# Kernel optimization log

Hardware: AMD Instinct MI355X
Metric: run time of the kernel (lower is better)

## Reference

```python
import jax, jax.numpy as jnp
import numpy as np

B, SQ, SKV, D = 32, 1024, 8192, 64

def setup_inputs() -> dict:
    key = jax.random.key(0)
    kq, kk, kv = jax.random.split(key, 3)
    return {
        "q_local": jax.random.normal(kq, (B, SQ, D), dtype=jnp.float32),
        "k_local": jax.random.normal(kk, (B, SKV, D), dtype=jnp.float32),
        "v_local": jax.random.normal(kv, (B, SKV, D), dtype=jnp.float32),
    }

def reference(q_local, k_local, v_local):
    # Ring attention with online softmax over all ranks' K/V blocks is
    # mathematically identical to unscaled softmax(Q K^T) V over the full KV.
    scores = jnp.einsum("bqd,bkd->bqk", q_local, k_local)  # [B, SQ, SKV]
    weights = jax.nn.softmax(scores, axis=-1)              # stable (max-subtract)
    out = jnp.einsum("bqk,bkd->bqd", weights, v_local)
    return out.astype(q_local.dtype)
```

## Files before the change

### kernel.cpp

```cpp
#include <hip/hip_runtime.h>


#define NBATCH 32
#define SQL 1024
#define SKVL 8192
#define DH 64
#define BM 128
#define BN 64
#define KSTR 72
#define VSTR 72

typedef _Float16 half8 __attribute__((ext_vector_type(8)));
typedef __fp16 fp16x2 __attribute__((ext_vector_type(2)));
typedef float floatx16 __attribute__((ext_vector_type(16)));
typedef float floatx4 __attribute__((ext_vector_type(4)));
typedef unsigned int uint4v __attribute__((ext_vector_type(4)));
typedef unsigned int uint2v __attribute__((ext_vector_type(2)));

union F8U { uint4v u; half8 h; };

#if __has_builtin(__builtin_amdgcn_exp2f)
#define EXP2F(x) __builtin_amdgcn_exp2f(x)
#else
#define EXP2F(x) exp2f(x)
#endif

static __device__ __forceinline__ unsigned pk2(float a, float b) {
#if __has_builtin(__builtin_amdgcn_cvt_pkrtz)
  fp16x2 h = __builtin_amdgcn_cvt_pkrtz(a, b);
  return __builtin_bit_cast(unsigned, h);
#else
  union { _Float16 h[2]; unsigned u; } r;
  r.h[0] = (_Float16)a; r.h[1] = (_Float16)b; return r.u;
#endif
}

#if __has_builtin(__builtin_amdgcn_permlane32_swap)
#define HAVE_PL32 1
static __device__ __forceinline__ void pl32(unsigned& a, unsigned& b) {
  uint2v r = __builtin_amdgcn_permlane32_swap(a, b, false, false);
  a = r[0]; b = r[1];
}
#else
#define HAVE_PL32 0
#endif

template<int NSPLIT>
__global__ __launch_bounds__(256, 3)
void ring_attn(const float* __restrict__ q, const float* __restrict__ k,
               const float* __restrict__ v, float* __restrict__ out,
               float* __restrict__ pO, float* __restrict__ pM, float* __restrict__ pL)
{
  constexpr int NT = SKVL / NSPLIT / BN;
  __shared__ _Float16 Kl[2][BN * KSTR];
  __shared__ _Float16 Vt[2][DH * VSTR];

  const int tid  = threadIdx.x;
  const int lane = tid & 63;
  const int wv   = tid >> 6;
  const int l31  = lane & 31;
  const int hb   = lane >> 5;
  const int b8   = hb * 8;

  int split, batch, qb;
  if (NSPLIT == 4) {
    split = blockIdx.x & 3;
    batch = (blockIdx.x >> 2) & 31;
    qb    = blockIdx.x >> 7;
  } else {
    split = 0;
    batch = blockIdx.x & 31;
    qb    = blockIdx.x >> 5;
  }

  const float* kp = k + ((size_t)batch * SKVL + (size_t)split * (SKVL / NSPLIT)) * DH;
  const float* vp = v + ((size_t)batch * SKVL + (size_t)split * (SKVL / NSPLIT)) * DH;

  const float* qp = q + ((size_t)batch * SQL + qb * BM + wv * 32 + l31) * DH;
  half8 qf[4];
#pragma unroll
  for (int kt = 0; kt < 4; ++kt) {
    float4 a = *(const float4*)(qp + kt * 16 + b8);
    float4 c = *(const float4*)(qp + kt * 16 + b8 + 4);
    float xs[8] = {a.x, a.y, a.z, a.w, c.x, c.y, c.z, c.w};
#pragma unroll
    for (int j = 0; j < 8; ++j)
      qf[kt][j] = (_Float16)(xs[j] * 1.44269504088896340736f);
  }

  const int krt = tid >> 4;
  const int kc  = (tid & 15) * 4;
  const int vnr = 2 * (tid & 31);
  const int vcg = 8 * (tid >> 5);

  float4 gk[4], ga0, ga1, gb0, gb1;
#pragma unroll
  for (int it = 0; it < 4; ++it)
    gk[it] = *(const float4*)(kp + (size_t)(krt + it * 16) * DH + kc);
  ga0 = *(const float4*)(vp + (size_t)vnr * DH + vcg);
  ga1 = *(const float4*)(vp + (size_t)vnr * DH + vcg + 4);
  gb0 = *(const float4*)(vp + (size_t)(vnr + 1) * DH + vcg);
  gb1 = *(const float4*)(vp + (size_t)(vnr + 1) * DH + vcg + 4);

  floatx16 accO[2];
#pragma unroll
  for (int i = 0; i < 2; ++i)
#pragma unroll
    for (int r = 0; r < 16; ++r) accO[i][r] = 0.f;
  float m_run = -3.0e38f, l_run = 0.f;

  int buf = 0;
  for (int tile = 0; tile < NT; ++tile) {
    _Float16* Kb = Kl[buf];
    _Float16* Vb = Vt[buf];

#pragma unroll
    for (int it = 0; it < 4; ++it) {
      uint2 w2 = make_uint2(pk2(gk[it].x, gk[it].y), pk2(gk[it].z, gk[it].w));
      *(uint2*)&Kb[(krt + it * 16) * KSTR + kc] = w2;
    }
    {
      float av[8] = {ga0.x, ga0.y, ga0.z, ga0.w, ga1.x, ga1.y, ga1.z, ga1.w};
      float bv[8] = {gb0.x, gb0.y, gb0.z, gb0.w, gb1.x, gb1.y, gb1.z, gb1.w};
#pragma unroll
      for (int i = 0; i < 8; ++i)
        *(unsigned*)&Vb[(vcg + i) * VSTR + vnr] = pk2(av[i], bv[i]);
    }
    __syncthreads();

    if (tile + 1 < NT) {
      const float* kn = kp + (size_t)(tile + 1) * BN * DH;
      const float* vn = vp + (size_t)(tile + 1) * BN * DH;
#pragma unroll
      for (int it = 0; it < 4; ++it)
        gk[it] = *(const float4*)(kn + (size_t)(krt + it * 16) * DH + kc);
      ga0 = *(const float4*)(vn + (size_t)vnr * DH + vcg);
      ga1 = *(const float4*)(vn + (size_t)vnr * DH + vcg + 4);
      gb0 = *(const float4*)(vn + (size_t)(vnr + 1) * DH + vcg);
      gb1 = *(const float4*)(vn + (size_t)(vnr + 1) * DH + vcg + 4);
    }

    floatx16 st[2];
#pragma unroll
    for (int t = 0; t < 2; ++t)
#pragma unroll
      for (int r = 0; r < 16; ++r) st[t][r] = 0.f;
#pragma unroll
    for (int kt = 0; kt < 4; ++kt) {
#pragma unroll
      for (int t = 0; t < 2; ++t) {
        half8 kf = *(const half8*)&Kb[(t * 32 + l31) * KSTR + kt * 16 + b8];
        st[t] = __builtin_amdgcn_mfma_f32_32x32x16_f16(kf, qf[kt], st[t], 0, 0, 0);
      }
    }

    float mx = -3.0e38f;
#pragma unroll
    for (int t = 0; t < 2; ++t)
#pragma unroll
      for (int r = 0; r < 16; ++r) mx = fmaxf(mx, st[t][r]);
    mx = fmaxf(mx, __shfl_xor(mx, 32, 64));
    float m_new = fmaxf(m_run, mx);
    float alpha = EXP2F(m_run - m_new);
    m_run = m_new;
    float sum = 0.f;
#pragma unroll
    for (int t = 0; t < 2; ++t)
#pragma unroll
      for (int r = 0; r < 16; ++r) {
        float p = EXP2F(st[t][r] - m_new);
        st[t][r] = p;
        sum += p;
      }
    sum += __shfl_xor(sum, 32, 64);
    l_run = alpha * l_run + sum;

    if (__any(alpha != 1.0f)) {
#pragma unroll
      for (int r = 0; r < 16; ++r) {
        int row = (r & 3) + 8 * (r >> 2) + 4 * hb;
        float ar = __shfl(alpha, row, 64);
        accO[0][r] *= ar;
        accO[1][r] *= ar;
      }
    }

#pragma unroll
    for (int t = 0; t < 2; ++t) {
      unsigned P01 = pk2(st[t][0],  st[t][1]);
      unsigned P23 = pk2(st[t][2],  st[t][3]);
      unsigned P45 = pk2(st[t][4],  st[t][5]);
      unsigned P67 = pk2(st[t][6],  st[t][7]);
      unsigned P89 = pk2(st[t][8],  st[t][9]);
      unsigned PAB = pk2(st[t][10], st[t][11]);
      unsigned PCD = pk2(st[t][12], st[t][13]);
      unsigned PEF = pk2(st[t][14], st[t][15]);
      F8U fe, fo;
#if HAVE_PL32
      pl32(P01, P45); fe.u[0] = P01; fe.u[2] = P45;
      pl32(P23, P67); fe.u[1] = P23; fe.u[3] = P67;
      pl32(P89, PCD); fo.u[0] = P89; fo.u[2] = PCD;
      pl32(PAB, PEF); fo.u[1] = PAB; fo.u[3] = PEF;
#else
      unsigned x01 = __shfl_xor(P01, 32, 64), x23 = __shfl_xor(P23, 32, 64);
      unsigned x45 = __shfl_xor(P45, 32, 64), x67 = __shfl_xor(P67, 32, 64);
      unsigned x89 = __shfl_xor(P89, 32, 64), xAB = __shfl_xor(PAB, 32, 64);
      unsigned xCD = __shfl_xor(PCD, 32, 64), xEF = __shfl_xor(PEF, 32, 64);
      fe.u = uint4v{hb ? x45 : P01, hb ? x67 : P23, hb ? P45 : x01, hb ? P67 : x23};
      fo.u = uint4v{hb ? xCD : P89, hb ? xEF : PAB, hb ? PCD : x89, hb ? PEF : xAB};
#endif
#pragma unroll
      for (int ds = 0; ds < 2; ++ds) {
        half8 vf0 = *(const half8*)&Vb[(ds * 32 + l31) * VSTR + (2 * t) * 16 + b8];
        accO[ds] = __builtin_amdgcn_mfma_f32_32x32x16_f16(fe.h, vf0, accO[ds], 0, 0, 0);
        half8 vf1 = *(const half8*)&Vb[(ds * 32 + l31) * VSTR + (2 * t + 1) * 16 + b8];
        accO[ds] = __builtin_amdgcn_mfma_f32_32x32x16_f16(fo.h, vf1, accO[ds], 0, 0, 0);
      }
    }
    buf ^= 1;
  }

  const int rowbase = batch * SQL + qb * BM + wv * 32;
  if (NSPLIT == 1) {
    float linv = 1.0f / l_run;
    float* op = out + (size_t)rowbase * DH;
#pragma unroll
    for (int r = 0; r < 16; ++r) {
      int row = (r & 3) + 8 * (r >> 2) + 4 * hb;
      float lr = __shfl(linv, row, 64);
      op[(size_t)row * DH + l31]      = accO[0][r] * lr;
      op[(size_t)row * DH + 32 + l31] = accO[1][r] * lr;
    }
  } else {
    float* po = pO + ((size_t)split * NBATCH * SQL + rowbase) * DH;
#pragma unroll
    for (int r = 0; r < 16; ++r) {
      int row = (r & 3) + 8 * (r >> 2) + 4 * hb;
      po[(size_t)row * DH + l31]      = accO[0][r];
      po[(size_t)row * DH + 32 + l31] = accO[1][r];
    }
    if (hb == 0) {
      pM[(size_t)split * NBATCH * SQL + rowbase + l31] = m_run;
      pL[(size_t)split * NBATCH * SQL + rowbase + l31] = l_run;
    }
  }
}

__global__ __launch_bounds__(256)
void merge4(const float* __restrict__ pO, const float* __restrict__ pM,
            const float* __restrict__ pL, float* __restrict__ out)
{
  const int i4   = blockIdx.x * 256 + threadIdx.x;
  const int rowg = i4 >> 4;
  const size_t PLANE4 = (size_t)NBATCH * SQL * DH / 4;
  const int    RPL    = NBATCH * SQL;
  float m0 = pM[rowg], m1 = pM[RPL + rowg], m2 = pM[2 * RPL + rowg], m3 = pM[3 * RPL + rowg];
  float mx = fmaxf(fmaxf(m0, m1), fmaxf(m2, m3));
  float w0 = EXP2F(m0 - mx), w1 = EXP2F(m1 - mx), w2 = EXP2F(m2 - mx), w3 = EXP2F(m3 - mx);
  float l = w0 * pL[rowg] + w1 * pL[RPL + rowg] + w2 * pL[2 * RPL + rowg] + w3 * pL[3 * RPL + rowg];
  float li = 1.0f / l;
  const floatx4* p0 = (const floatx4*)pO;
  floatx4 o0 = p0[i4], o1 = p0[PLANE4 + i4], o2 = p0[2 * PLANE4 + i4], o3 = p0[3 * PLANE4 + i4];
  floatx4 o;
#pragma unroll
  for (int j = 0; j < 4; ++j)
    o[j] = (w0 * o0[j] + w1 * o1[j] + w2 * o2[j] + w3 * o3[j]) * li;
  ((floatx4*)out)[i4] = o;
}

extern "C" void kernel_launch(void* const* d_in, const int* in_sizes, int n_in,
                              void* d_out, int out_size, void* d_ws, size_t ws_size,
                              hipStream_t stream) {
  (void)in_sizes; (void)n_in; (void)out_size;
  const float* q = (const float*)d_in[0];
  const float* k = (const float*)d_in[1];
  const float* v = (const float*)d_in[2];
  float* out = (float*)d_out;

  const size_t PLANE = (size_t)NBATCH * SQL * DH;
  const size_t RPL   = (size_t)NBATCH * SQL;
  const size_t need  = (4 * PLANE + 8 * RPL) * sizeof(float);

  if (ws_size >= need) {
    float* pO = (float*)d_ws;
    float* pM = pO + 4 * PLANE;
    float* pL = pM + 4 * RPL;
    ring_attn<4><<<dim3(1024), dim3(256), 0, stream>>>(q, k, v, nullptr, pO, pM, pL);
    merge4<<<dim3((NBATCH * SQL * DH) / 1024), dim3(256), 0, stream>>>(pO, pM, pL, out);
  } else {
    ring_attn<1><<<dim3(256), dim3(256), 0, stream>>>(q, k, v, out, nullptr, nullptr, nullptr);
  }
}
```

Before: 250.9 us.

## Split tile barrier so V stores overlap QK MFMAs, add setprio and tree reductions

New measurement: 245.2 us. -2.3%, faster.

```diff
diff --git a/kernel.cpp b/kernel.cpp
--- a/kernel.cpp
+++ b/kernel.cpp
@@ -24,6 +24,12 @@
 #else
 #define EXP2F(x) exp2f(x)
 #endif
+
+#define WGBAR() do {                                        \
+    asm volatile("s_waitcnt lgkmcnt(0)" ::: "memory");      \
+    __builtin_amdgcn_s_barrier();                           \
+    asm volatile("" ::: "memory");                          \
+  } while (0)
 
 static __device__ __forceinline__ unsigned pk2(float a, float b) {
 #if __has_builtin(__builtin_amdgcn_cvt_pkrtz)
@@ -119,6 +125,8 @@
       uint2 w2 = make_uint2(pk2(gk[it].x, gk[it].y), pk2(gk[it].z, gk[it].w));
       *(uint2*)&Kb[(krt + it * 16) * KSTR + kc] = w2;
     }
+    WGBAR();
+
     {
       float av[8] = {ga0.x, ga0.y, ga0.z, ga0.w, ga1.x, ga1.y, ga1.z, ga1.w};
       float bv[8] = {gb0.x, gb0.y, gb0.z, gb0.w, gb1.x, gb1.y, gb1.z, gb1.w};
@@ -126,7 +134,6 @@
       for (int i = 0; i < 8; ++i)
         *(unsigned*)&Vb[(vcg + i) * VSTR + vnr] = pk2(av[i], bv[i]);
     }
-    __syncthreads();
 
     if (tile + 1 < NT) {
       const float* kn = kp + (size_t)(tile + 1) * BN * DH;
@@ -145,6 +152,7 @@
     for (int t = 0; t < 2; ++t)
 #pragma unroll
       for (int r = 0; r < 16; ++r) st[t][r] = 0.f;
+    __builtin_amdgcn_s_setprio(1);
 #pragma unroll
     for (int kt = 0; kt < 4; ++kt) {
 #pragma unroll
@@ -153,26 +161,34 @@
         st[t] = __builtin_amdgcn_mfma_f32_32x32x16_f16(kf, qf[kt], st[t], 0, 0, 0);
       }
     }
-
-    float mx = -3.0e38f;
-#pragma unroll
-    for (int t = 0; t < 2; ++t)
-#pragma unroll
-      for (int r = 0; r < 16; ++r) mx = fmaxf(mx, st[t][r]);
-    mx = fmaxf(mx, __shfl_xor(mx, 32, 64));
+    __builtin_amdgcn_s_setprio(0);
+
+    float red[16];
+#pragma unroll
+    for (int r = 0; r < 16; ++r) red[r] = fmaxf(st[0][r], st[1][r]);
+#pragma unroll
+    for (int s = 8; s >= 1; s >>= 1)
+#pragma unroll
+      for (int r = 0; r < 8; ++r)
+        if (r < s) red[r] = fmaxf(red[r], red[r + s]);
+    float mx = fmaxf(red[0], __shfl_xor(red[0], 32, 64));
     float m_new = fmaxf(m_run, mx);
     float alpha = EXP2F(m_run - m_new);
     m_run = m_new;
-    float sum = 0.f;
 #pragma unroll
     for (int t = 0; t < 2; ++t)
 #pragma unroll
-      for (int r = 0; r < 16; ++r) {
-        float p = EXP2F(st[t][r] - m_new);
-        st[t][r] = p;
-        sum += p;
-      }
-    sum += __shfl_xor(sum, 32, 64);
+      for (int r = 0; r < 16; ++r)
+        st[t][r] = EXP2F(st[t][r] - m_new);
+    float sm[16];
+#pragma unroll
+    for (int r = 0; r < 16; ++r) sm[r] = st[0][r] + st[1][r];
+#pragma unroll
+    for (int s = 8; s >= 1; s >>= 1)
+#pragma unroll
+      for (int r = 0; r < 8; ++r)
+        if (r < s) sm[r] += sm[r + s];
+    float sum = sm[0] + __shfl_xor(sm[0], 32, 64);
     l_run = alpha * l_run + sum;
 
     if (__any(alpha != 1.0f)) {
@@ -185,6 +201,9 @@
       }
     }
 
+    WGBAR();
+
+    __builtin_amdgcn_s_setprio(1);
 #pragma unroll
     for (int t = 0; t < 2; ++t) {
       unsigned P01 = pk2(st[t][0],  st[t][1]);
@@ -217,6 +236,7 @@
         accO[ds] = __builtin_amdgcn_mfma_f32_32x32x16_f16(fo.h, vf1, accO[ds], 0, 0, 0);
       }
     }
+    __builtin_amdgcn_s_setprio(0);
     buf ^= 1;
   }
 
```
